# Optimization experiments

Hardware: AMD Instinct MI355X
Metric: run time of the kernel (lower is better)

The kernel has to match this reference:

```python
import jax, jax.numpy as jnp
import numpy as np

B, C, S, H = 8, 10, 512, 768
WIN = 5  # window_size


def setup_inputs() -> dict:
    key = jax.random.key(0)
    ks = jax.random.split(key, 12)
    def rn(k, shape, s=0.02):
        return jax.random.normal(k, shape, jnp.float32) * s
    return {
        "token_embeddings": jax.random.normal(ks[0], (B * C, S, H), jnp.float32),
        "w_tok": rn(ks[1], (1, H)), "b_tok": jnp.zeros((1,), jnp.float32),
        "w_sum": rn(ks[2], (H, H)), "b_sum": jnp.zeros((H,), jnp.float32),
        "w_proj": rn(ks[3], (2 * H, H)), "b_proj": jnp.zeros((2 * H,), jnp.float32),
        "w_ih_f": rn(ks[4], (4 * H, H)), "w_hh_f": rn(ks[5], (4 * H, H)),
        "b_ih_f": jnp.zeros((4 * H,), jnp.float32), "b_hh_f": jnp.zeros((4 * H,), jnp.float32),
        "w_ih_b": rn(ks[6], (4 * H, H)), "w_hh_b": rn(ks[7], (4 * H, H)),
        "b_ih_b": jnp.zeros((4 * H,), jnp.float32), "b_hh_b": jnp.zeros((4 * H,), jnp.float32),
        "w_cls": rn(ks[8], (1, 2 * H)), "b_cls": jnp.zeros((1,), jnp.float32),
        "num_chunks": C,
    }


def _lstm_dir(x, w_ih, w_hh, b_ih, b_hh, reverse):
    # x: [B, T, H]; PyTorch gate order i, f, g, o
    Bs, T, Hin = x.shape
    Hh = w_hh.shape[1]
    xs = jnp.einsum('bth,gh->btg', x, w_ih) + b_ih  # precompute input projections
    xs = jnp.swapaxes(xs, 0, 1)  # [T, B, 4H]
    if reverse:
        xs = xs[::-1]
    def step(carry, xt):
        h, c = carry
        g = xt + h @ w_hh.T + b_hh
        i, f, gg, o = jnp.split(g, 4, axis=-1)
        c = jax.nn.sigmoid(f) * c + jax.nn.sigmoid(i) * jnp.tanh(gg)
        h = jax.nn.sigmoid(o) * jnp.tanh(c)
        return (h, c), h
    init = (jnp.zeros((Bs, Hh), x.dtype), jnp.zeros((Bs, Hh), x.dtype))
    _, hs = jax.lax.scan(step, init, xs)
    if reverse:
        hs = hs[::-1]
    return jnp.swapaxes(hs, 0, 1)  # [B, T, Hh]


def reference(token_embeddings, w_tok, b_tok, w_sum, b_sum, w_proj, b_proj,
              w_ih_f, w_hh_f, b_ih_f, b_hh_f, w_ih_b, w_hh_b, b_ih_b, b_hh_b,
              w_cls, b_cls, num_chunks):
    BC, S_, H_ = token_embeddings.shape
    Bsz = BC // num_chunks
    # token_predictor + sigmoid -> [BC, S]
    scores = jax.nn.sigmoid(jnp.einsum('bsh,oh->bs', token_embeddings, w_tok) + b_tok[0])
    pad = WIN // 2
    padded = jnp.pad(scores, ((0, 0), (pad, pad)))
    cs = jnp.pad(jnp.cumsum(padded, axis=1), ((0, 0), (1, 0)))
    windowed = (cs[:, WIN:] - cs[:, :-WIN]) / WIN  # [BC, S]
    # summarize: score-weighted sum over tokens, then linear
    weighted = jnp.einsum('bsh,bs->bh', token_embeddings, windowed)
    summ = weighted @ w_sum.T + b_sum  # [BC, H]
    summ = summ.reshape(Bsz, num_chunks, H_).mean(axis=1)
    summ = summ @ w_proj.T + b_proj  # [B, 2H]
    # CLS-token embeddings per chunk -> biLSTM
    chunk = token_embeddings[:, 0, :].reshape(Bsz, num_chunks, H_)
    hf = _lstm_dir(chunk, w_ih_f, w_hh_f, b_ih_f, b_hh_f, False)
    hb = _lstm_dir(chunk, w_ih_b, w_hh_b, b_ih_b, b_hh_b, True)
    glob = jnp.concatenate([hf, hb], axis=-1)[:, -1, :]  # [B, 2H]
    combined = glob + summ
    class_probs = jax.nn.sigmoid(combined @ w_cls.T + b_cls)[:, 0]
    return (class_probs, windowed, summ)
```

## Files before the change

kernel.cpp:

```cpp
#include <hip/hip_runtime.h>

namespace {

constexpr int Bsz = 8, NC = 10, BC = 80, S = 512, H = 768, G4 = 3072, H2 = 1536;
constexpr int FA_CH = 64, FA_ROWS = 8, FA_STG = 12;
constexpr int FA_BLK = BC * FA_CH;
constexpr int XF_BLK = 960, XB_BLK = 96;
constexpr int XG_BLK = XF_BLK + XB_BLK;
constexpr int NBACK = 96;
constexpr int HP = 772;

typedef float f32x4 __attribute__((ext_vector_type(4)));

__device__ __forceinline__ float sigm(float x){ return 1.0f/(1.0f + __expf(-x)); }
__device__ __forceinline__ float tanh_fast(float x){ return 1.0f - 2.0f/(__expf(2.0f*x) + 1.0f); }
__device__ __forceinline__ float vdot(f32x4 a, f32x4 b){ f32x4 m = a*b; return m.x+m.y+m.z+m.w; }
__device__ __forceinline__ float hsum(f32x4 a){ return (a.x+a.y)+(a.z+a.w); }
__device__ __forceinline__ float wred(float v){
  #pragma unroll
  for (int m = 32; m; m >>= 1) v += __shfl_xor(v, m, 64);
  return v;
}

__device__ __forceinline__ void coh_load6(f32x4 (&d)[6],
    const f32x4* p0, const f32x4* p1, const f32x4* p2,
    const f32x4* p3, const f32x4* p4, const f32x4* p5){
  asm volatile(
    "global_load_dwordx4 %0, %6, off sc0 sc1\n\t"
    "global_load_dwordx4 %1, %7, off sc0 sc1\n\t"
    "global_load_dwordx4 %2, %8, off sc0 sc1\n\t"
    "global_load_dwordx4 %3, %9, off sc0 sc1\n\t"
    "global_load_dwordx4 %4, %10, off sc0 sc1\n\t"
    "global_load_dwordx4 %5, %11, off sc0 sc1\n\t"
    "s_waitcnt vmcnt(0)"
    : "=&v"(d[0]), "=&v"(d[1]), "=&v"(d[2]), "=&v"(d[3]), "=&v"(d[4]), "=&v"(d[5])
    : "v"(p0), "v"(p1), "v"(p2), "v"(p3), "v"(p4), "v"(p5)
    : "memory");
}
__device__ __forceinline__ void coh_store1(float* p, float v){
  asm volatile("global_store_dword %0, %1, off sc0 sc1" :: "v"(p), "v"(v) : "memory");
}

__global__ __launch_bounds__(256) void k_fa(
    const float* __restrict__ tok, const float* __restrict__ w_tok,
    const float* __restrict__ b_tok, float* __restrict__ win_out,
    float* __restrict__ wpart, unsigned* __restrict__ ctr){
  __shared__ float smemF[FA_STG * HP];
  __shared__ float scr[FA_STG];
  __shared__ float wsh[FA_ROWS];
  int blk = blockIdx.x, tid = threadIdx.x;

  if (blk == 0 && tid < 16) ctr[tid] = 0;

  int bc = blk >> 6, ch = blk & 63;
  int s0 = ch * FA_ROWS;
  #pragma unroll
  for (int i = 0; i < 9; i++){
    int f = i * 256 + tid;
    int row = f / 192, c4 = f % 192;
    int gs = s0 - 2 + row;
    if (gs >= 0 && gs < S)
      *(f32x4*)&smemF[row * HP + c4 * 4] =
        *(const f32x4*)&tok[((size_t)bc * S + gs) * H + c4 * 4];
  }
  __syncthreads();
  if (tid < 192){
    int r = tid >> 4, e = tid & 15;
    int gs = s0 - 2 + r;
    const f32x4* wq = (const f32x4*)w_tok;
    f32x4 a4 = {0.f, 0.f, 0.f, 0.f};
    #pragma unroll
    for (int i = 0; i < 12; i++){
      int k = e + 16 * i;
      a4 += *(const f32x4*)&smemF[r * HP + k * 4] * wq[k];
    }
    float acc = hsum(a4);
    acc += __shfl_xor(acc, 1, 64);
    acc += __shfl_xor(acc, 2, 64);
    acc += __shfl_xor(acc, 4, 64);
    acc += __shfl_xor(acc, 8, 64);
    if (e == 0) scr[r] = (gs >= 0 && gs < S) ? sigm(acc + b_tok[0]) : 0.f;
  }
  __syncthreads();
  if (tid < FA_ROWS){
    float w = (scr[tid] + scr[tid+1] + scr[tid+2] + scr[tid+3] + scr[tid+4]) * 0.2f;
    wsh[tid] = w;
    win_out[(size_t)bc * S + s0 + tid] = w;
  }
  __syncthreads();
  if (tid < 192){
    f32x4 acc = {0.f, 0.f, 0.f, 0.f};
    #pragma unroll
    for (int i = 0; i < FA_ROWS; i++){
      float w = wsh[i];
      f32x4 a = *(const f32x4*)&smemF[(i + 2) * HP + tid * 4];
      acc += a * w;
    }
    *(f32x4*)&wpart[((size_t)ch * BC + bc) * H + tid * 4] = acc;
  }
}

__global__ __launch_bounds__(256) void k_xg(
    const float* __restrict__ tok,
    const float* __restrict__ w_ih_f, const float* __restrict__ b_ih_f, const float* __restrict__ b_hh_f,
    const float* __restrict__ w_ih_b, const float* __restrict__ b_ih_b, const float* __restrict__ b_hh_b,
    float* __restrict__ xg, float* __restrict__ gbwd){
  __shared__ float smemX[8 * HP];
  int blk = blockIdx.x, tid = threadIdx.x;
  bool fwd = (blk < XF_BLK);
  int rblk, base_bc = 0;
  const float *w, *bi, *bh; float* outp;
  if (fwd){ rblk = blk / 10; base_bc = (blk % 10) * 8; w = w_ih_f; bi = b_ih_f; bh = b_hh_f; outp = xg; }
  else    { rblk = blk - XF_BLK;                      w = w_ih_b; bi = b_ih_b; bh = b_hh_b; outp = gbwd; }
  #pragma unroll
  for (int i = 0; i < 6; i++){
    int f = i * 256 + tid;
    int bl = f / 192, c4 = f % 192;
    size_t bc = fwd ? (size_t)(base_bc + bl) : ((size_t)bl * NC + NC - 1);
    *(f32x4*)&smemX[bl * HP + c4 * 4] = *(const f32x4*)&tok[bc * (size_t)S * H + c4 * 4];
  }
  __syncthreads();
  {
    int bl = tid & 7, rl = tid >> 3;
    int r = rblk * 32 + rl;
    const f32x4* wr = (const f32x4*)(w + (size_t)r * H);
    f32x4 a4 = {0.f, 0.f, 0.f, 0.f};
    #pragma unroll 8
    for (int k = 0; k < 192; k++)
      a4 += *(const f32x4*)&smemX[bl * HP + k * 4] * wr[k];
    int ob = fwd ? (base_bc + bl) : bl;
    outp[(size_t)ob * G4 + r] = hsum(a4) + bi[r] + bh[r];
  }
}

struct BackArgs {
  const float *w_sum, *b_sum, *w_proj, *b_proj;
  const float *w_hh, *xg, *gbwd, *w_cls, *b_cls, *wpart;
  float *wmean, *s1, *summ_out, *hx, *cls_out;
  unsigned *ctr;
};

__global__ __launch_bounds__(256) void k_back(BackArgs A){
  __shared__ float smem[37696];
  float* w_sh  = smem;
  float* h_sh  = smem + 24704;
  float* a_sh  = smem + 30880;
  float* c_sh  = smem + 37056;
  float* g_sh  = smem + 37120;
  float* pg_sh = smem + 37376;
  int tid = threadIdx.x, lane = tid & 63, wv = tid >> 6, blkx = blockIdx.x;

  auto gbar = [&](int slot){
    asm volatile("s_waitcnt vmcnt(0)" ::: "memory");
    __syncthreads();
    if (tid == 0){
      __hip_atomic_fetch_add(&A.ctr[slot], 1u, __ATOMIC_RELAXED, __HIP_MEMORY_SCOPE_AGENT);
      while (__hip_atomic_load(&A.ctr[slot], __ATOMIC_RELAXED, __HIP_MEMORY_SCOPE_AGENT) < (unsigned)NBACK)
        __builtin_amdgcn_s_sleep(1);
    }
    __syncthreads();
  };

  auto stage6 = [&](float* dst, const float* src){
    const f32x4* s4 = (const f32x4*)src;
    f32x4 d[6];
    coh_load6(d, s4 + tid, s4 + 256 + tid, s4 + 512 + tid,
                 s4 + 768 + tid, s4 + 1024 + tid, s4 + 1280 + tid);
    #pragma unroll
    for (int i = 0; i < 6; i++){
      int f = i * 256 + tid, b = f / 192, j4 = f % 192;
      *(f32x4*)&dst[b * HP + j4 * 4] = d[i];
    }
  };

  #pragma unroll
  for (int i = 0; i < 24; i++){
    int f = i * 256 + tid;
    int lr = f / 192, k = f % 192;
    int g = lr & 3, jl = lr >> 2;
    int r = g * H + blkx * 8 + jl;
    *(f32x4*)&w_sh[lr * HP + k * 4] = *(const f32x4*)&A.w_hh[(size_t)r * H + k * 4];
  }

  auto do_step = [&](int t){
    int b = tid & 7, lr = tid >> 3;
    int g = lr & 3, jl = lr >> 2;
    int r = g * H + blkx * 8 + jl;
    float xgv = A.xg[((size_t)b * NC + t) * G4 + r];
    const f32x4* wr = (const f32x4*)&w_sh[lr * HP];
    const f32x4* hb = (const f32x4*)&h_sh[b * HP];
    f32x4 a4 = {0.f, 0.f, 0.f, 0.f};
    #pragma unroll 8
    for (int k = 0; k < 192; k++)
      a4 += wr[k] * hb[k];
    g_sh[jl * 32 + g * 8 + b] = hsum(a4) + xgv;
    __syncthreads();
    if (tid < 64){
      int jj = tid >> 3, b2 = tid & 7;
      float gi = g_sh[jj*32 + b2],      gf = g_sh[jj*32 + 8 + b2];
      float gg = g_sh[jj*32 + 16 + b2], go = g_sh[jj*32 + 24 + b2];
      float c = sigm(gf) * c_sh[tid] + sigm(gi) * tanh_fast(gg);
      c_sh[tid] = c;
      coh_store1(&A.hx[(t & 1) * (Bsz*H) + b2 * H + blkx * 8 + jj],
                 sigm(go) * tanh_fast(c));
    }
  };

  {
    int out = tid >> 2, ps = tid & 3;
    int idx = blkx * 64 + out;
    int b = idx / H, hh = idx % H;
    float acc = 0.f;
    for (int p = ps * 16; p < ps * 16 + 16; p++)
      #pragma unroll
      for (int c = 0; c < NC; c++)
        acc += A.wpart[((size_t)p * BC + b * NC + c) * H + hh];
    pg_sh[out * 5 + ps] = acc;
  }
  __syncthreads();
  if (tid < 64){
    float acc = pg_sh[tid*5] + pg_sh[tid*5+1] + pg_sh[tid*5+2] + pg_sh[tid*5+3];
    coh_store1(&A.wmean[blkx * 64 + tid], acc * 0.1f);
    int jl = tid >> 3, b2 = tid & 7, j = blkx * 8 + jl;
    const float* gp = A.xg + (size_t)(b2 * NC) * G4;
    float c = sigm(gp[j]) * tanh_fast(gp[2*H + j]);
    c_sh[tid] = c;
    coh_store1(&A.hx[b2 * H + j], sigm(gp[3*H + j]) * tanh_fast(c));
  }
  gbar(0);

  stage6(a_sh, A.wmean);
  stage6(h_sh, A.hx);
  __syncthreads();
  {
    int out = tid >> 2, q = tid & 3;
    int ol = out >> 3, b = out & 7;
    int o = blkx * 8 + ol;
    const f32x4* wq = (const f32x4*)(A.w_sum + (size_t)o * H) + q * 48;
    f32x4 a4 = {0.f, 0.f, 0.f, 0.f};
    #pragma unroll 8
    for (int k = 0; k < 48; k++)
      a4 += *(const f32x4*)&a_sh[b * HP + (q * 48 + k) * 4] * wq[k];
    float acc = hsum(a4);
    acc += __shfl_xor(acc, 1, 64);
    acc += __shfl_xor(acc, 2, 64);
    if (q == 0) coh_store1(&A.s1[(size_t)b * H + o], acc + A.b_sum[o]);
  }
  do_step(1);
  gbar(1);

  stage6(a_sh, A.s1);
  stage6(h_sh, A.hx + Bsz*H);
  __syncthreads();
  {
    int out = tid >> 1, hf = tid & 1;
    int ol = out >> 3, b = out & 7;
    int o = blkx * 16 + ol;
    const f32x4* wq = (const f32x4*)(A.w_proj + (size_t)o * H) + hf * 96;
    f32x4 a4 = {0.f, 0.f, 0.f, 0.f};
    #pragma unroll 8
    for (int k = 0; k < 96; k++)
      a4 += *(const f32x4*)&a_sh[b * HP + (hf * 96 + k) * 4] * wq[k];
    float acc = hsum(a4);
    acc += __shfl_xor(acc, 1, 64);
    if (hf == 0) coh_store1(&A.summ_out[(size_t)b * H2 + o], acc + A.b_proj[o]);
  }
  do_step(2);
  gbar(2);

  for (int t = 3; t <= 9; t++){
    stage6(h_sh, A.hx + ((t - 1) & 1) * (Bsz*H));
    __syncthreads();
    do_step(t);
    gbar(t);
  }

  if (blkx == 0){
    float* comb = smem;
    {
      f32x4 d[6];
      const f32x4* h4 = (const f32x4*)(A.hx + Bsz*H);
      coh_load6(d, h4 + tid, h4 + 256 + tid, h4 + 512 + tid,
                   h4 + 768 + tid, h4 + 1024 + tid, h4 + 1280 + tid);
      #pragma unroll
      for (int i = 0; i < 6; i++){
        int f = i * 256 + tid, b = f / 192, e = (f % 192) * 4;
        *(f32x4*)&comb[b * H2 + e] = d[i];
      }
      #pragma unroll
      for (int u = 0; u < 6; u++){
        int f = u * 256 + tid;
        int b = f / 192, e = (f % 192) * 4;
        f32x4 gi = *(const f32x4*)&A.gbwd[(size_t)b * G4 + e];
        f32x4 gg = *(const f32x4*)&A.gbwd[(size_t)b * G4 + 2*H + e];
        f32x4 go = *(const f32x4*)&A.gbwd[(size_t)b * G4 + 3*H + e];
        f32x4 hb;
        hb.x = sigm(go.x) * tanh_fast(sigm(gi.x) * tanh_fast(gg.x));
        hb.y = sigm(go.y) * tanh_fast(sigm(gi.y) * tanh_fast(gg.y));
        hb.z = sigm(go.z) * tanh_fast(sigm(gi.z) * tanh_fast(gg.z));
        hb.w = sigm(go.w) * tanh_fast(sigm(gi.w) * tanh_fast(gg.w));
        *(f32x4*)&comb[b * H2 + H + e] = hb;
      }
    }
    __syncthreads();
    {
      f32x4 d[6];
      const f32x4* s4 = (const f32x4*)A.summ_out;
      coh_load6(d, s4 + tid, s4 + 256 + tid, s4 + 512 + tid,
                   s4 + 768 + tid, s4 + 1024 + tid, s4 + 1280 + tid);
      #pragma unroll
      for (int i = 0; i < 6; i++) *(f32x4*)&comb[(i * 256 + tid) * 4] += d[i];
      coh_load6(d, s4 + 1536 + tid, s4 + 1792 + tid, s4 + 2048 + tid,
                   s4 + 2304 + tid, s4 + 2560 + tid, s4 + 2816 + tid);
      #pragma unroll
      for (int i = 0; i < 6; i++) *(f32x4*)&comb[(1536 + i * 256 + tid) * 4] += d[i];
    }
    __syncthreads();
    for (int b = wv; b < Bsz; b += 4){
      const f32x4* c4 = (const f32x4*)&comb[b * H2];
      const f32x4* wc = (const f32x4*)A.w_cls;
      f32x4 a4 = {0.f, 0.f, 0.f, 0.f};
      #pragma unroll
      for (int k = 0; k < 6; k++)
        a4 += c4[lane + 64*k] * wc[lane + 64*k];
      float acc = wred(hsum(a4));
      if (lane == 0) A.cls_out[b] = sigm(acc + A.b_cls[0]);
    }
  }
}

}

extern "C" void kernel_launch(void* const* d_in, const int* in_sizes, int n_in,
                              void* d_out, int out_size, void* d_ws, size_t ws_size,
                              hipStream_t stream) {
  const float* tok    = (const float*)d_in[0];
  const float* w_tok  = (const float*)d_in[1];
  const float* b_tok  = (const float*)d_in[2];
  const float* w_sum  = (const float*)d_in[3];
  const float* b_sum  = (const float*)d_in[4];
  const float* w_proj = (const float*)d_in[5];
  const float* b_proj = (const float*)d_in[6];
  const float* w_ih_f = (const float*)d_in[7];
  const float* w_hh_f = (const float*)d_in[8];
  const float* b_ih_f = (const float*)d_in[9];
  const float* b_hh_f = (const float*)d_in[10];
  const float* w_ih_b = (const float*)d_in[11];
  const float* b_ih_b = (const float*)d_in[13];
  const float* b_hh_b = (const float*)d_in[14];
  const float* w_cls  = (const float*)d_in[15];
  const float* b_cls  = (const float*)d_in[16];

  float* out      = (float*)d_out;
  float* cls_out  = out;
  float* win_out  = out + 8;
  float* summ_out = out + 8 + BC * S;

  float* ws     = (float*)d_ws;
  float* wpart  = ws;
  float* wmean  = wpart + (size_t)FA_CH * BC * H;
  float* s1     = wmean + Bsz * H;
  float* xg     = s1 + Bsz * H;
  float* gbwd   = xg + (size_t)BC * G4;
  float* hx     = gbwd + (size_t)Bsz * G4;
  unsigned* ctr = (unsigned*)(hx + 2 * Bsz * H);

  k_fa<<<FA_BLK, 256, 0, stream>>>(tok, w_tok, b_tok, win_out, wpart, ctr);
  k_xg<<<XG_BLK, 256, 0, stream>>>(tok, w_ih_f, b_ih_f, b_hh_f,
                                   w_ih_b, b_ih_b, b_hh_b, xg, gbwd);

  BackArgs ba;
  ba.w_sum = w_sum; ba.b_sum = b_sum; ba.w_proj = w_proj; ba.b_proj = b_proj;
  ba.w_hh = w_hh_f; ba.xg = xg; ba.gbwd = gbwd; ba.w_cls = w_cls; ba.b_cls = b_cls;
  ba.wpart = wpart; ba.wmean = wmean; ba.s1 = s1; ba.summ_out = summ_out;
  ba.hx = hx; ba.cls_out = cls_out; ba.ctr = ctr;

  void* params[] = { &ba };
  hipLaunchCooperativeKernel(reinterpret_cast<void*>(k_back),
                             dim3(NBACK), dim3(256), params, 0, stream);
}
```

Baseline: 185.1 us.

## Merge front kernels, use hierarchical grid barrier, prefetch next-step gate inputs

Fuses the window-attention and LSTM input-projection kernels into a single launch so they share one grid and one kernel boundary. The grid barrier in the recurrent kernel becomes two-level: blocks arrive on per-group counters spaced apart in memory, and the last arrival of each group bumps a global counter. This is meant to reduce atomic contention on one address. The precomputed input gate value for the next timestep is loaded before the barrier so its latency overlaps the wait. In exchange, the counter region grows and must be zeroed by block 0 of the front kernel.

```diff
diff --git a/kernel.cpp b/kernel.cpp
--- a/kernel.cpp
+++ b/kernel.cpp
@@ -6,15 +6,15 @@
 constexpr int FA_CH = 64, FA_ROWS = 8, FA_STG = 12;
 constexpr int FA_BLK = BC * FA_CH;
 constexpr int XF_BLK = 960, XB_BLK = 96;
-constexpr int XG_BLK = XF_BLK + XB_BLK;
+constexpr int FRONT_BLK = FA_BLK + XF_BLK + XB_BLK;
 constexpr int NBACK = 96;
 constexpr int HP = 772;
+constexpr int CTR_N = 1600;
 
 typedef float f32x4 __attribute__((ext_vector_type(4)));
 
 __device__ __forceinline__ float sigm(float x){ return 1.0f/(1.0f + __expf(-x)); }
 __device__ __forceinline__ float tanh_fast(float x){ return 1.0f - 2.0f/(__expf(2.0f*x) + 1.0f); }
-__device__ __forceinline__ float vdot(f32x4 a, f32x4 b){ f32x4 m = a*b; return m.x+m.y+m.z+m.w; }
 __device__ __forceinline__ float hsum(f32x4 a){ return (a.x+a.y)+(a.z+a.w); }
 __device__ __forceinline__ float wred(float v){
   #pragma unroll
@@ -41,83 +41,82 @@
   asm volatile("global_store_dword %0, %1, off sc0 sc1" :: "v"(p), "v"(v) : "memory");
 }
 
-__global__ __launch_bounds__(256) void k_fa(
+__global__ __launch_bounds__(256) void k_front(
     const float* __restrict__ tok, const float* __restrict__ w_tok,
     const float* __restrict__ b_tok, float* __restrict__ win_out,
-    float* __restrict__ wpart, unsigned* __restrict__ ctr){
+    float* __restrict__ wpart,
+    const float* __restrict__ w_ih_f, const float* __restrict__ b_ih_f, const float* __restrict__ b_hh_f,
+    const float* __restrict__ w_ih_b, const float* __restrict__ b_ih_b, const float* __restrict__ b_hh_b,
+    float* __restrict__ xg, float* __restrict__ gbwd, unsigned* __restrict__ ctr){
   __shared__ float smemF[FA_STG * HP];
   __shared__ float scr[FA_STG];
   __shared__ float wsh[FA_ROWS];
   int blk = blockIdx.x, tid = threadIdx.x;
 
-  if (blk == 0 && tid < 16) ctr[tid] = 0;
-
-  int bc = blk >> 6, ch = blk & 63;
-  int s0 = ch * FA_ROWS;
-  #pragma unroll
-  for (int i = 0; i < 9; i++){
-    int f = i * 256 + tid;
-    int row = f / 192, c4 = f % 192;
-    int gs = s0 - 2 + row;
-    if (gs >= 0 && gs < S)
-      *(f32x4*)&smemF[row * HP + c4 * 4] =
-        *(const f32x4*)&tok[((size_t)bc * S + gs) * H + c4 * 4];
-  }
-  __syncthreads();
-  if (tid < 192){
-    int r = tid >> 4, e = tid & 15;
-    int gs = s0 - 2 + r;
-    const f32x4* wq = (const f32x4*)w_tok;
-    f32x4 a4 = {0.f, 0.f, 0.f, 0.f};
+  if (blk == 0) for (int i = tid; i < CTR_N; i += 256) ctr[i] = 0;
+
+  if (blk < FA_BLK){
+    int bc = blk >> 6, ch = blk & 63;
+    int s0 = ch * FA_ROWS;
     #pragma unroll
-    for (int i = 0; i < 12; i++){
-      int k = e + 16 * i;
-      a4 += *(const f32x4*)&smemF[r * HP + k * 4] * wq[k];
-    }
-    float acc = hsum(a4);
-    acc += __shfl_xor(acc, 1, 64);
-    acc += __shfl_xor(acc, 2, 64);
-    acc += __shfl_xor(acc, 4, 64);
-    acc += __shfl_xor(acc, 8, 64);
-    if (e == 0) scr[r] = (gs >= 0 && gs < S) ? sigm(acc + b_tok[0]) : 0.f;
-  }
-  __syncthreads();
-  if (tid < FA_ROWS){
-    float w = (scr[tid] + scr[tid+1] + scr[tid+2] + scr[tid+3] + scr[tid+4]) * 0.2f;
-    wsh[tid] = w;
-    win_out[(size_t)bc * S + s0 + tid] = w;
-  }
-  __syncthreads();
-  if (tid < 192){
-    f32x4 acc = {0.f, 0.f, 0.f, 0.f};
-    #pragma unroll
-    for (int i = 0; i < FA_ROWS; i++){
-      float w = wsh[i];
-      f32x4 a = *(const f32x4*)&smemF[(i + 2) * HP + tid * 4];
-      acc += a * w;
-    }
-    *(f32x4*)&wpart[((size_t)ch * BC + bc) * H + tid * 4] = acc;
-  }
-}
-
-__global__ __launch_bounds__(256) void k_xg(
-    const float* __restrict__ tok,
-    const float* __restrict__ w_ih_f, const float* __restrict__ b_ih_f, const float* __restrict__ b_hh_f,
-    const float* __restrict__ w_ih_b, const float* __restrict__ b_ih_b, const float* __restrict__ b_hh_b,
-    float* __restrict__ xg, float* __restrict__ gbwd){
-  __shared__ float smemX[8 * HP];
-  int blk = blockIdx.x, tid = threadIdx.x;
-  bool fwd = (blk < XF_BLK);
+    for (int i = 0; i < 9; i++){
+      int f = i * 256 + tid;
+      int row = f / 192, c4 = f % 192;
+      int gs = s0 - 2 + row;
+      if (gs >= 0 && gs < S)
+        *(f32x4*)&smemF[row * HP + c4 * 4] =
+          *(const f32x4*)&tok[((size_t)bc * S + gs) * H + c4 * 4];
+    }
+    __syncthreads();
+    if (tid < 192){
+      int r = tid >> 4, e = tid & 15;
+      int gs = s0 - 2 + r;
+      const f32x4* wq = (const f32x4*)w_tok;
+      f32x4 a4 = {0.f, 0.f, 0.f, 0.f};
+      #pragma unroll
+      for (int i = 0; i < 12; i++){
+        int k = e + 16 * i;
+        a4 += *(const f32x4*)&smemF[r * HP + k * 4] * wq[k];
+      }
+      float acc = hsum(a4);
+      acc += __shfl_xor(acc, 1, 64);
+      acc += __shfl_xor(acc, 2, 64);
+      acc += __shfl_xor(acc, 4, 64);
+      acc += __shfl_xor(acc, 8, 64);
+      if (e == 0) scr[r] = (gs >= 0 && gs < S) ? sigm(acc + b_tok[0]) : 0.f;
+    }
+    __syncthreads();
+    if (tid < FA_ROWS){
+      float w = (scr[tid] + scr[tid+1] + scr[tid+2] + scr[tid+3] + scr[tid+4]) * 0.2f;
+      wsh[tid] = w;
+      win_out[(size_t)bc * S + s0 + tid] = w;
+    }
+    __syncthreads();
+    if (tid < 192){
+      f32x4 acc = {0.f, 0.f, 0.f, 0.f};
+      #pragma unroll
+      for (int i = 0; i < FA_ROWS; i++){
+        float w = wsh[i];
+        f32x4 a = *(const f32x4*)&smemF[(i + 2) * HP + tid * 4];
+        acc += a * w;
+      }
+      *(f32x4*)&wpart[((size_t)ch * BC + bc) * H + tid * 4] = acc;
+    }
+    return;
+  }
+
+  int xb = blk - FA_BLK;
+  bool fwd = (xb < XF_BLK);
   int rblk, base_bc = 0;
   const float *w, *bi, *bh; float* outp;
-  if (fwd){ rblk = blk / 10; base_bc = (blk % 10) * 8; w = w_ih_f; bi = b_ih_f; bh = b_hh_f; outp = xg; }
-  else    { rblk = blk - XF_BLK;                      w = w_ih_b; bi = b_ih_b; bh = b_hh_b; outp = gbwd; }
+  if (fwd){ rblk = xb / 10; base_bc = (xb % 10) * 8; w = w_ih_f; bi = b_ih_f; bh = b_hh_f; outp = xg; }
+  else    { rblk = xb - XF_BLK;                      w = w_ih_b; bi = b_ih_b; bh = b_hh_b; outp = gbwd; }
   #pragma unroll
   for (int i = 0; i < 6; i++){
     int f = i * 256 + tid;
     int bl = f / 192, c4 = f % 192;
     size_t bc = fwd ? (size_t)(base_bc + bl) : ((size_t)bl * NC + NC - 1);
-    *(f32x4*)&smemX[bl * HP + c4 * 4] = *(const f32x4*)&tok[bc * (size_t)S * H + c4 * 4];
+    *(f32x4*)&smemF[bl * HP + c4 * 4] = *(const f32x4*)&tok[bc * (size_t)S * H + c4 * 4];
   }
   __syncthreads();
   {
@@ -127,7 +126,7 @@
     f32x4 a4 = {0.f, 0.f, 0.f, 0.f};
     #pragma unroll 8
     for (int k = 0; k < 192; k++)
-      a4 += *(const f32x4*)&smemX[bl * HP + k * 4] * wr[k];
+      a4 += *(const f32x4*)&smemF[bl * HP + k * 4] * wr[k];
     int ob = fwd ? (base_bc + bl) : bl;
     outp[(size_t)ob * G4 + r] = hsum(a4) + bi[r] + bh[r];
   }
@@ -154,8 +153,13 @@
     asm volatile("s_waitcnt vmcnt(0)" ::: "memory");
     __syncthreads();
     if (tid == 0){
-      __hip_atomic_fetch_add(&A.ctr[slot], 1u, __ATOMIC_RELAXED, __HIP_MEMORY_SCOPE_AGENT);
-      while (__hip_atomic_load(&A.ctr[slot], __ATOMIC_RELAXED, __HIP_MEMORY_SCOPE_AGENT) < (unsigned)NBACK)
+      unsigned* base = A.ctr + slot * 160;
+      int grp = blkx / 12;
+      unsigned old = __hip_atomic_fetch_add(&base[grp * 16], 1u,
+                        __ATOMIC_RELAXED, __HIP_MEMORY_SCOPE_AGENT);
+      if (old == 11u)
+        __hip_atomic_fetch_add(&base[128], 1u, __ATOMIC_RELAXED, __HIP_MEMORY_SCOPE_AGENT);
+      while (__hip_atomic_load(&base[128], __ATOMIC_RELAXED, __HIP_MEMORY_SCOPE_AGENT) < 8u)
         __builtin_amdgcn_s_sleep(1);
     }
     __syncthreads();
@@ -182,18 +186,19 @@
     *(f32x4*)&w_sh[lr * HP + k * 4] = *(const f32x4*)&A.w_hh[(size_t)r * H + k * 4];
   }
 
-  auto do_step = [&](int t){
-    int b = tid & 7, lr = tid >> 3;
-    int g = lr & 3, jl = lr >> 2;
-    int r = g * H + blkx * 8 + jl;
-    float xgv = A.xg[((size_t)b * NC + t) * G4 + r];
-    const f32x4* wr = (const f32x4*)&w_sh[lr * HP];
-    const f32x4* hb = (const f32x4*)&h_sh[b * HP];
+  int sb = tid & 7, slr = tid >> 3;
+  int sjl = slr >> 2, sg = slr & 3;
+  int sr = sg * H + blkx * 8 + sjl;
+  size_t xgrow = (size_t)sb * NC;
+
+  auto do_step = [&](int t, float xgv){
+    const f32x4* wr = (const f32x4*)&w_sh[slr * HP];
+    const f32x4* hb = (const f32x4*)&h_sh[sb * HP];
     f32x4 a4 = {0.f, 0.f, 0.f, 0.f};
     #pragma unroll 8
     for (int k = 0; k < 192; k++)
       a4 += wr[k] * hb[k];
-    g_sh[jl * 32 + g * 8 + b] = hsum(a4) + xgv;
+    g_sh[sjl * 32 + sg * 8 + sb] = hsum(a4) + xgv;
     __syncthreads();
     if (tid < 64){
       int jj = tid >> 3, b2 = tid & 7;
@@ -227,6 +232,7 @@
     c_sh[tid] = c;
     coh_store1(&A.hx[b2 * H + j], sigm(gp[3*H + j]) * tanh_fast(c));
   }
+  float xgv = A.xg[(xgrow + 1) * G4 + sr];
   gbar(0);
 
   stage6(a_sh, A.wmean);
@@ -246,7 +252,8 @@
     acc += __shfl_xor(acc, 2, 64);
     if (q == 0) coh_store1(&A.s1[(size_t)b * H + o], acc + A.b_sum[o]);
   }
-  do_step(1);
+  do_step(1, xgv);
+  xgv = A.xg[(xgrow + 2) * G4 + sr];
   gbar(1);
 
   stage6(a_sh, A.s1);
@@ -265,13 +272,15 @@
     acc += __shfl_xor(acc, 1, 64);
     if (hf == 0) coh_store1(&A.summ_out[(size_t)b * H2 + o], acc + A.b_proj[o]);
   }
-  do_step(2);
+  do_step(2, xgv);
+  xgv = A.xg[(xgrow + 3) * G4 + sr];
   gbar(2);
 
   for (int t = 3; t <= 9; t++){
     stage6(h_sh, A.hx + ((t - 1) & 1) * (Bsz*H));
     __syncthreads();
-    do_step(t);
+    do_step(t, xgv);
+    if (t < 9) xgv = A.xg[(xgrow + t + 1) * G4 + sr];
     gbar(t);
   }
 
@@ -365,9 +374,9 @@
   float* hx     = gbwd + (size_t)Bsz * G4;
   unsigned* ctr = (unsigned*)(hx + 2 * Bsz * H);
 
-  k_fa<<<FA_BLK, 256, 0, stream>>>(tok, w_tok, b_tok, win_out, wpart, ctr);
-  k_xg<<<XG_BLK, 256, 0, stream>>>(tok, w_ih_f, b_ih_f, b_hh_f,
-                                   w_ih_b, b_ih_b, b_hh_b, xg, gbwd);
+  k_front<<<FRONT_BLK, 256, 0, stream>>>(tok, w_tok, b_tok, win_out, wpart,
+                                         w_ih_f, b_ih_f, b_hh_f,
+                                         w_ih_b, b_ih_b, b_hh_b, xg, gbwd, ctr);
 
   BackArgs ba;
   ba.w_sum = w_sum; ba.b_sum = b_sum; ba.w_proj = w_proj; ba.b_proj = b_proj;
```

Measured after the change: 177.8 us, median of 2. 4.0% less time.
